# Kernel optimization log

Measured on AMD Instinct MI355X. Metric: run time of the kernel, lower is better.

The kernel has to match this reference:

```python
import jax, jax.numpy as jnp
import numpy as np

B, T, N = 16, 2048, 1024
SPIKE_RATE = 0.02


def setup_inputs() -> dict:
    key = jax.random.key(0)
    k1, k2 = jax.random.split(key)
    u = jax.random.uniform(k1, (B, T, N), dtype=jnp.float32)
    output_spikes = (u < SPIKE_RATE).astype(jnp.float32)
    target_cv = jax.random.uniform(k2, (N,), dtype=jnp.float32)
    return {"output_spikes": output_spikes, "target_cv": target_cv}


def reference(output_spikes, target_cv):
    # Flatten (batch[, patterns], time) into one long trial-concatenated train per neuron,
    # matching output_spikes[:, :, n].reshape(-1) in the torch loop.
    n_neurons = output_spikes.shape[-1]
    s = output_spikes.reshape(-1, n_neurons)          # (Ttot, N)
    Ttot = s.shape[0]
    m = s > 0                                          # spike mask
    times = jnp.arange(Ttot, dtype=jnp.float32)[:, None]

    # Previous spike time at each position via exclusive cumulative max of spike times.
    st = jnp.where(m, times, -1.0)                     # (Ttot, N)
    cmax = jax.lax.cummax(st, axis=0)
    prev = jnp.concatenate([jnp.full((1, n_neurons), -1.0, st.dtype), cmax[:-1]], axis=0)

    # ISI gap at every spike that has a predecessor: gap = t - prev_spike_time.
    gmask = m & (prev >= 0.0)
    gaps = jnp.where(gmask, times - prev, 0.0)

    k = jnp.sum(m, axis=0).astype(jnp.float32)         # spike count per neuron
    n_isi = k - 1.0                                    # number of ISIs
    sum_g = jnp.sum(gaps, axis=0)
    sum_g2 = jnp.sum(gaps * gaps, axis=0)

    mean_isi = sum_g / jnp.maximum(n_isi, 1.0)
    # torch.Tensor.std is unbiased (divide by n_isi - 1)
    var = (sum_g2 - n_isi * mean_isi * mean_isi) / jnp.maximum(n_isi - 1.0, 1.0)
    std = jnp.sqrt(jnp.maximum(var, 0.0))

    # NaN in torch corresponds here to: <3 spikes or mean_isi <= 0 -> excluded from loss.
    valid = (k >= 3.0) & (mean_isi > 0.0)
    cv = jnp.where(valid, std / jnp.where(mean_isi > 0.0, mean_isi, 1.0), 0.0)
    sq = jnp.where(valid, (cv - target_cv) ** 2, 0.0)
    nvalid = jnp.sum(valid.astype(jnp.float32))
    return jnp.where(nvalid > 0.0, jnp.sum(sq) / jnp.maximum(nvalid, 1.0), 0.0)
```

## Files before the change

### kernel.cpp

```cpp
#include <hip/hip_runtime.h>
#include <math.h>

#define TTOT   32768
#define NNEUR  1024
#define NCHUNK 256
#define SUBLEN 32
#define NC4    (NNEUR / 4)
#define LBATCH 8

typedef float f32x4 __attribute__((ext_vector_type(4)));

struct SegState { float cnt, first, last, g2; };

__device__ __forceinline__ SegState seg_combine(const SegState& a, const SegState& b) {
    if (a.cnt == 0.0f) return b;
    if (b.cnt == 0.0f) return a;
    SegState r;
    float gap = b.first - a.last;
    r.cnt   = a.cnt + b.cnt;
    r.first = a.first;
    r.last  = b.last;
    r.g2    = a.g2 + b.g2 + gap * gap;
    return r;
}

__global__ __launch_bounds__(256) void k_scan(const float* __restrict__ s,
                                              float4* __restrict__ wstate) {
    const int tid  = threadIdx.x;
    const int ccol = tid & 63;
    const int ysl  = tid >> 6;
    const int col4 = blockIdx.x * 64 + ccol;
    const int t0   = blockIdx.y * 128 + ysl * SUBLEN;

    const f32x4* s4 = reinterpret_cast<const f32x4*>(s);

    float cnt[4]   = {0.f, 0.f, 0.f, 0.f};
    float first[4] = {-1.f, -1.f, -1.f, -1.f};
    float last[4]  = {-1.f, -1.f, -1.f, -1.f};
    float g2[4]    = {0.f, 0.f, 0.f, 0.f};

    for (int g = 0; g < SUBLEN / LBATCH; ++g) {
        f32x4 v[LBATCH];
        #pragma unroll
        for (int i = 0; i < LBATCH; ++i)
            v[i] = __builtin_nontemporal_load(
                &s4[(size_t)(t0 + g * LBATCH + i) * NC4 + col4]);

        #pragma unroll
        for (int i = 0; i < LBATCH; ++i) {
            const float tt = (float)(t0 + g * LBATCH + i);
            #pragma unroll
            for (int j = 0; j < 4; ++j) {
                if (v[i][j] > 0.0f) {
                    if (cnt[j] > 0.0f) {
                        float gp = tt - last[j];
                        g2[j] += gp * gp;
                    } else {
                        first[j] = tt;
                    }
                    last[j] = tt;
                    cnt[j] += 1.0f;
                }
            }
        }
    }

    __shared__ float4 lds[4][64][4];
    #pragma unroll
    for (int j = 0; j < 4; ++j)
        lds[ysl][ccol][j] = make_float4(cnt[j], first[j], last[j], g2[j]);
    __syncthreads();

    if (ysl == 0) {
        #pragma unroll
        for (int j = 0; j < 4; ++j) {
            float4 a = lds[0][ccol][j];
            SegState st = {a.x, a.y, a.z, a.w};
            #pragma unroll
            for (int y = 1; y < 4; ++y) {
                float4 b = lds[y][ccol][j];
                SegState sb = {b.x, b.y, b.z, b.w};
                st = seg_combine(st, sb);
            }
            wstate[(size_t)blockIdx.y * NNEUR + col4 * 4 + j] =
                make_float4(st.cnt, st.first, st.last, st.g2);
        }
    }
}

__global__ __launch_bounds__(256) void k_combine(const float4* __restrict__ wstate,
                                                 const float* __restrict__ target,
                                                 float* __restrict__ outsq,
                                                 float* __restrict__ outvalid) {
    const int tid  = threadIdx.x;
    const int lane = tid & 63;
    const int w    = tid >> 6;
    const int n    = blockIdx.x * 4 + w;

    SegState st = {0.f, -1.f, -1.f, 0.f};
    #pragma unroll
    for (int j = 0; j < NCHUNK / 64; ++j) {
        int c = lane * (NCHUNK / 64) + j;
        float4 a = wstate[(size_t)c * NNEUR + n];
        SegState sb = {a.x, a.y, a.z, a.w};
        st = seg_combine(st, sb);
    }
    for (int off = 1; off < 64; off <<= 1) {
        SegState o;
        o.cnt   = __shfl_down(st.cnt,   off);
        o.first = __shfl_down(st.first, off);
        o.last  = __shfl_down(st.last,  off);
        o.g2    = __shfl_down(st.g2,    off);
        if ((lane & (2 * off - 1)) == 0) st = seg_combine(st, o);
    }

    if (lane == 0) {
        float k     = st.cnt;
        float n_isi = k - 1.0f;
        float sum_g = (k > 0.0f) ? (st.last - st.first) : 0.0f;
        float mean  = sum_g / fmaxf(n_isi, 1.0f);
        float var   = (st.g2 - n_isi * mean * mean) / fmaxf(n_isi - 1.0f, 1.0f);
        float sd    = sqrtf(fmaxf(var, 0.0f));
        bool valid  = (k >= 3.0f) && (mean > 0.0f);
        float cv    = valid ? sd / mean : 0.0f;
        float d     = cv - target[n];
        outsq[n]    = valid ? d * d : 0.0f;
        outvalid[n] = valid ? 1.0f : 0.0f;
    }
}

__global__ __launch_bounds__(256) void k_reduce(const float* __restrict__ outsq,
                                                const float* __restrict__ outvalid,
                                                float* __restrict__ out) {
    const int tid = threadIdx.x;
    float s = 0.f, v = 0.f;
    for (int i = tid; i < NNEUR; i += 256) {
        s += outsq[i];
        v += outvalid[i];
    }
    for (int off = 32; off > 0; off >>= 1) {
        s += __shfl_down(s, off);
        v += __shfl_down(v, off);
    }
    __shared__ float ls[4], lv[4];
    const int w = tid >> 6;
    if ((tid & 63) == 0) { ls[w] = s; lv[w] = v; }
    __syncthreads();
    if (tid == 0) {
        float S = ls[0] + ls[1] + ls[2] + ls[3];
        float V = lv[0] + lv[1] + lv[2] + lv[3];
        out[0] = (V > 0.0f) ? S / fmaxf(V, 1.0f) : 0.0f;
    }
}

extern "C" void kernel_launch(void* const* d_in, const int* in_sizes, int n_in,
                              void* d_out, int out_size, void* d_ws, size_t ws_size,
                              hipStream_t stream) {
    const float* spikes = (const float*)d_in[0];
    const float* target = (const float*)d_in[1];
    float* out = (float*)d_out;

    char* wsb = (char*)d_ws;
    float4* wstate   = (float4*)wsb;
    float*  outsq    = (float*)(wsb + (size_t)NCHUNK * NNEUR * sizeof(float4));
    float*  outvalid = outsq + NNEUR;

    dim3 g1(NNEUR / 256, NCHUNK);
    k_scan<<<g1, 256, 0, stream>>>(spikes, wstate);
    k_combine<<<NNEUR / 4, 256, 0, stream>>>(wstate, target, outsq, outvalid);
    k_reduce<<<1, 256, 0, stream>>>(outsq, outvalid, out);
}
```

Baseline: 35.61 us.

## Retile scan so each block covers full rows across all neurons, 512 time chunks

```diff
diff --git a/kernel.cpp b/kernel.cpp
--- a/kernel.cpp
+++ b/kernel.cpp
@@ -1,12 +1,12 @@
 #include <hip/hip_runtime.h>
 #include <math.h>
 
-#define TTOT   32768
-#define NNEUR  1024
-#define NCHUNK 256
-#define SUBLEN 32
-#define NC4    (NNEUR / 4)
-#define LBATCH 8
+#define TTOT            32768
+#define NNEUR           1024
+#define NC4             256
+#define ROWS_PER_WAVE   16
+#define ROWS_PER_BLOCK  64
+#define NCHUNK          512
 
 typedef float f32x4 __attribute__((ext_vector_type(4)));
 
@@ -27,62 +27,74 @@
 __global__ __launch_bounds__(256) void k_scan(const float* __restrict__ s,
                                               float4* __restrict__ wstate) {
     const int tid  = threadIdx.x;
-    const int ccol = tid & 63;
-    const int ysl  = tid >> 6;
-    const int col4 = blockIdx.x * 64 + ccol;
-    const int t0   = blockIdx.y * 128 + ysl * SUBLEN;
+    const int lane = tid & 63;
+    const int w    = tid >> 6;
+    const int rowbase = blockIdx.x * ROWS_PER_BLOCK + w * ROWS_PER_WAVE;
 
     const f32x4* s4 = reinterpret_cast<const f32x4*>(s);
 
-    float cnt[4]   = {0.f, 0.f, 0.f, 0.f};
-    float first[4] = {-1.f, -1.f, -1.f, -1.f};
-    float last[4]  = {-1.f, -1.f, -1.f, -1.f};
-    float g2[4]    = {0.f, 0.f, 0.f, 0.f};
-
-    for (int g = 0; g < SUBLEN / LBATCH; ++g) {
-        f32x4 v[LBATCH];
-        #pragma unroll
-        for (int i = 0; i < LBATCH; ++i)
-            v[i] = __builtin_nontemporal_load(
-                &s4[(size_t)(t0 + g * LBATCH + i) * NC4 + col4]);
-
-        #pragma unroll
-        for (int i = 0; i < LBATCH; ++i) {
-            const float tt = (float)(t0 + g * LBATCH + i);
+    float cnt[4][4], first[4][4], last[4][4], g2[4][4];
+    #pragma unroll
+    for (int p = 0; p < 4; ++p)
+        #pragma unroll
+        for (int k = 0; k < 4; ++k) {
+            cnt[p][k] = 0.f; first[p][k] = -1.f; last[p][k] = -1.f; g2[p][k] = 0.f;
+        }
+
+    for (int rb = 0; rb < ROWS_PER_WAVE; rb += 2) {
+        f32x4 v[2][4];
+        #pragma unroll
+        for (int r = 0; r < 2; ++r)
             #pragma unroll
-            for (int j = 0; j < 4; ++j) {
-                if (v[i][j] > 0.0f) {
-                    if (cnt[j] > 0.0f) {
-                        float gp = tt - last[j];
-                        g2[j] += gp * gp;
-                    } else {
-                        first[j] = tt;
+            for (int p = 0; p < 4; ++p)
+                v[r][p] = s4[(size_t)(rowbase + rb + r) * NC4 + p * 64 + lane];
+
+        #pragma unroll
+        for (int r = 0; r < 2; ++r) {
+            const float tt = (float)(rowbase + rb + r);
+            #pragma unroll
+            for (int p = 0; p < 4; ++p)
+                #pragma unroll
+                for (int k = 0; k < 4; ++k) {
+                    if (v[r][p][k] > 0.0f) {
+                        if (cnt[p][k] > 0.0f) {
+                            float gp = tt - last[p][k];
+                            g2[p][k] += gp * gp;
+                        } else {
+                            first[p][k] = tt;
+                        }
+                        last[p][k] = tt;
+                        cnt[p][k] += 1.0f;
                     }
-                    last[j] = tt;
-                    cnt[j] += 1.0f;
                 }
-            }
-        }
-    }
-
-    __shared__ float4 lds[4][64][4];
-    #pragma unroll
-    for (int j = 0; j < 4; ++j)
-        lds[ysl][ccol][j] = make_float4(cnt[j], first[j], last[j], g2[j]);
+        }
+    }
+
+    __shared__ float lcnt[4][4][256], lfirst[4][4][256], llast[4][4][256], lg2[4][4][256];
+    #pragma unroll
+    for (int p = 0; p < 4; ++p) {
+        const int col = p * 64 + lane;
+        #pragma unroll
+        for (int k = 0; k < 4; ++k) {
+            lcnt  [w][k][col] = cnt[p][k];
+            lfirst[w][k][col] = first[p][k];
+            llast [w][k][col] = last[p][k];
+            lg2   [w][k][col] = g2[p][k];
+        }
+    }
     __syncthreads();
 
-    if (ysl == 0) {
-        #pragma unroll
-        for (int j = 0; j < 4; ++j) {
-            float4 a = lds[0][ccol][j];
-            SegState st = {a.x, a.y, a.z, a.w};
+    {
+        const int col = tid;
+        #pragma unroll
+        for (int k = 0; k < 4; ++k) {
+            SegState st = {lcnt[0][k][col], lfirst[0][k][col], llast[0][k][col], lg2[0][k][col]};
             #pragma unroll
             for (int y = 1; y < 4; ++y) {
-                float4 b = lds[y][ccol][j];
-                SegState sb = {b.x, b.y, b.z, b.w};
-                st = seg_combine(st, sb);
+                SegState b = {lcnt[y][k][col], lfirst[y][k][col], llast[y][k][col], lg2[y][k][col]};
+                st = seg_combine(st, b);
             }
-            wstate[(size_t)blockIdx.y * NNEUR + col4 * 4 + j] =
+            wstate[(size_t)blockIdx.x * NNEUR + col * 4 + k] =
                 make_float4(st.cnt, st.first, st.last, st.g2);
         }
     }
@@ -95,37 +107,62 @@
     const int tid  = threadIdx.x;
     const int lane = tid & 63;
     const int w    = tid >> 6;
-    const int n    = blockIdx.x * 4 + w;
-
-    SegState st = {0.f, -1.f, -1.f, 0.f};
-    #pragma unroll
-    for (int j = 0; j < NCHUNK / 64; ++j) {
-        int c = lane * (NCHUNK / 64) + j;
-        float4 a = wstate[(size_t)c * NNEUR + n];
-        SegState sb = {a.x, a.y, a.z, a.w};
-        st = seg_combine(st, sb);
+    const int n0   = blockIdx.x * 4;
+
+    SegState st[4];
+    #pragma unroll
+    for (int k = 0; k < 4; ++k) st[k] = {0.f, -1.f, -1.f, 0.f};
+
+    #pragma unroll
+    for (int j = 0; j < 2; ++j) {
+        const int c = tid * 2 + j;
+        #pragma unroll
+        for (int k = 0; k < 4; ++k) {
+            float4 a = wstate[(size_t)c * NNEUR + n0 + k];
+            SegState sb = {a.x, a.y, a.z, a.w};
+            st[k] = seg_combine(st[k], sb);
+        }
     }
     for (int off = 1; off < 64; off <<= 1) {
-        SegState o;
-        o.cnt   = __shfl_down(st.cnt,   off);
-        o.first = __shfl_down(st.first, off);
-        o.last  = __shfl_down(st.last,  off);
-        o.g2    = __shfl_down(st.g2,    off);
-        if ((lane & (2 * off - 1)) == 0) st = seg_combine(st, o);
-    }
-
+        #pragma unroll
+        for (int k = 0; k < 4; ++k) {
+            SegState o;
+            o.cnt   = __shfl_down(st[k].cnt,   off);
+            o.first = __shfl_down(st[k].first, off);
+            o.last  = __shfl_down(st[k].last,  off);
+            o.g2    = __shfl_down(st[k].g2,    off);
+            if ((lane & (2 * off - 1)) == 0) st[k] = seg_combine(st[k], o);
+        }
+    }
+    __shared__ float4 lw[4][4];
     if (lane == 0) {
-        float k     = st.cnt;
-        float n_isi = k - 1.0f;
-        float sum_g = (k > 0.0f) ? (st.last - st.first) : 0.0f;
+        #pragma unroll
+        for (int k = 0; k < 4; ++k)
+            lw[w][k] = make_float4(st[k].cnt, st[k].first, st[k].last, st[k].g2);
+    }
+    __syncthreads();
+
+    if (tid < 4) {
+        const int k = tid;
+        float4 a = lw[0][k];
+        SegState s0 = {a.x, a.y, a.z, a.w};
+        #pragma unroll
+        for (int y = 1; y < 4; ++y) {
+            float4 b = lw[y][k];
+            SegState sb = {b.x, b.y, b.z, b.w};
+            s0 = seg_combine(s0, sb);
+        }
+        float kk    = s0.cnt;
+        float n_isi = kk - 1.0f;
+        float sum_g = (kk > 0.0f) ? (s0.last - s0.first) : 0.0f;
         float mean  = sum_g / fmaxf(n_isi, 1.0f);
-        float var   = (st.g2 - n_isi * mean * mean) / fmaxf(n_isi - 1.0f, 1.0f);
+        float var   = (s0.g2 - n_isi * mean * mean) / fmaxf(n_isi - 1.0f, 1.0f);
         float sd    = sqrtf(fmaxf(var, 0.0f));
-        bool valid  = (k >= 3.0f) && (mean > 0.0f);
+        bool valid  = (kk >= 3.0f) && (mean > 0.0f);
         float cv    = valid ? sd / mean : 0.0f;
-        float d     = cv - target[n];
-        outsq[n]    = valid ? d * d : 0.0f;
-        outvalid[n] = valid ? 1.0f : 0.0f;
+        float d     = cv - target[n0 + k];
+        outsq[n0 + k]    = valid ? d * d : 0.0f;
+        outvalid[n0 + k] = valid ? 1.0f : 0.0f;
     }
 }
 
@@ -165,8 +202,7 @@
     float*  outsq    = (float*)(wsb + (size_t)NCHUNK * NNEUR * sizeof(float4));
     float*  outvalid = outsq + NNEUR;
 
-    dim3 g1(NNEUR / 256, NCHUNK);
-    k_scan<<<g1, 256, 0, stream>>>(spikes, wstate);
+    k_scan<<<NCHUNK, 256, 0, stream>>>(spikes, wstate);
     k_combine<<<NNEUR / 4, 256, 0, stream>>>(wstate, target, outsq, outvalid);
     k_reduce<<<1, 256, 0, stream>>>(outsq, outvalid, out);
 }
```

New measurement: 68.09 us. 91.2% more time.
